# Kernel tuning notes

Hardware: AMD Instinct MI355X
Metric: run time of the kernel (lower is better)

The kernel has to match this reference:

```python
import jax, jax.numpy as jnp
import numpy as np

N_NODES = 100000
N_EDGES = 3200000


def setup_inputs() -> dict:
    key = jax.random.key(0)
    ks = jax.random.split(key, 20)
    x = jax.random.normal(ks[0], (N_NODES, 3), dtype=jnp.float32)
    edge_index = jax.random.randint(ks[1], (2, N_EDGES), 0, N_NODES, dtype=jnp.int64)

    def w(k, shape, fan_in):
        return jax.random.normal(k, shape, dtype=jnp.float32) * (1.0 / np.sqrt(fan_in))

    return {
        "x": x, "edge_index": edge_index,
        # layer 1: in=3, out=16, heads=2
        "W1": w(ks[2], (3, 32), 3), "a_src1": w(ks[3], (2, 16), 16), "a_dst1": w(ks[4], (2, 16), 16), "b1": jnp.zeros((32,), jnp.float32),
        # layer 2: in=32, out=16, heads=2
        "W2": w(ks[5], (32, 32), 32), "a_src2": w(ks[6], (2, 16), 16), "a_dst2": w(ks[7], (2, 16), 16), "b2": jnp.zeros((32,), jnp.float32),
        # layer 3: in=32, out=16, heads=1
        "W3": w(ks[8], (32, 16), 32), "a_src3": w(ks[9], (1, 16), 16), "a_dst3": w(ks[10], (1, 16), 16), "b3": jnp.zeros((16,), jnp.float32),
        # output linear 16 -> 1
        "Wout": w(ks[11], (16, 1), 16), "bout": jnp.zeros((1,), jnp.float32),
    }


def gat_layer(x, src, dst, W, a_src, a_dst, b, heads, ch, n):
    # h: [N, H, C]
    h = (x @ W).reshape(n, heads, ch)
    alpha_src = jnp.sum(h * a_src[None], axis=-1)  # [N, H]
    alpha_dst = jnp.sum(h * a_dst[None], axis=-1)  # [N, H]
    e = jax.nn.leaky_relu(alpha_src[src] + alpha_dst[dst], 0.2)  # [E, H]
    # segment softmax over incoming edges of each dst node
    m = jax.ops.segment_max(e, dst, num_segments=n)
    m = jnp.where(jnp.isfinite(m), m, 0.0)
    ex = jnp.exp(e - jax.lax.stop_gradient(m)[dst])
    s = jax.ops.segment_sum(ex, dst, num_segments=n)
    alpha = ex / (s[dst] + 1e-16)  # [E, H]
    out = jax.ops.segment_sum(h[src] * alpha[:, :, None], dst, num_segments=n)  # [N, H, C]
    return out.reshape(n, heads * ch) + b


def reference(x, edge_index, W1, a_src1, a_dst1, b1, W2, a_src2, a_dst2, b2,
              W3, a_src3, a_dst3, b3, Wout, bout):
    n = x.shape[0]
    loops = jnp.arange(n, dtype=edge_index.dtype)
    src = jnp.concatenate([edge_index[0], loops])  # PyG add_self_loops=True
    dst = jnp.concatenate([edge_index[1], loops])
    h = jax.nn.elu(gat_layer(x, src, dst, W1, a_src1, a_dst1, b1, 2, 16, n))
    h = jax.nn.elu(gat_layer(h, src, dst, W2, a_src2, a_dst2, b2, 2, 16, n))
    h = jax.nn.elu(gat_layer(h, src, dst, W3, a_src3, a_dst3, b3, 1, 16, n))
    embeddings = h
    out = jax.nn.sigmoid(h @ Wout + bout)
    return out, embeddings
```

## Files before the change

kernel.cpp:

```cpp
#include <hip/hip_runtime.h>
#include <hip/hip_fp16.h>
#include <math.h>

#define TPB 256
#define PMAX 128
#define PSH 10
#define PW  1024
#define CHUNK 2048
#define KPT 8
#define PCAP 49152
#define PCSTR 16

__device__ __forceinline__ float leaky02(float x) { return x > 0.f ? x : 0.2f * x; }
__device__ __forceinline__ float eluf(float x) { return x > 0.f ? x : (__expf(x) - 1.f); }


__global__ void zero_kernel(int* __restrict__ p, int n) {
  int i = blockIdx.x * blockDim.x + threadIdx.x;
  if (i < n) p[i] = 0;
}

__global__ __launch_bounds__(256) void scatter_kernel(const int* __restrict__ src,
                                                      const int* __restrict__ dst,
                                                      int E, int n,
                                                      int* __restrict__ pcursor,
                                                      unsigned* __restrict__ pstage) {
  __shared__ int lcnt[4][PMAX];
  __shared__ int ltot[PMAX];
  __shared__ int lscan[PMAX];
  __shared__ int lbase[PMAX];
  __shared__ int wtot;
  __shared__ unsigned slab[CHUNK];
  int t = threadIdx.x;
  int wid = t >> 6;
  int lane = t & 63;
  int Etot = E + n;
  int c0 = blockIdx.x * CHUNK;
  if (c0 >= Etot) return;
  int c1 = min(c0 + CHUNK, Etot);
  for (int j = t; j < 4 * PMAX; j += TPB) ((int*)lcnt)[j] = 0;

  int dd[KPT], ss[KPT];
  bool vv[KPT];
#pragma unroll
  for (int k = 0; k < KPT; ++k) {
    int idx = c0 + t + k * TPB;
    vv[k] = idx < c1;
    if (vv[k]) {
      if (idx < E) { ss[k] = src[idx]; dd[k] = dst[idx]; }
      else         { ss[k] = dd[k] = idx - E; }
    } else { ss[k] = 0; dd[k] = 0; }
  }
  __syncthreads();
#pragma unroll
  for (int k = 0; k < KPT; ++k)
    if (vv[k]) atomicAdd(&lcnt[wid][dd[k] >> PSH], 1);
  __syncthreads();
  int tot = 0, x = 0;
  if (t < PMAX) {
    int a0 = lcnt[0][t], a1 = lcnt[1][t], a2 = lcnt[2][t], a3 = lcnt[3][t];
    tot = a0 + a1 + a2 + a3;
    ltot[t] = tot;
    lcnt[0][t] = 0; lcnt[1][t] = a0; lcnt[2][t] = a0 + a1; lcnt[3][t] = a0 + a1 + a2;
    x = tot;
#pragma unroll
    for (int off = 1; off < 64; off <<= 1) {
      int u = __shfl_up(x, off);
      if (lane >= off) x += u;
    }
    if (t == 63) wtot = x;
  }
  __syncthreads();
  if (t < PMAX) {
    lscan[t] = x - tot + ((t >= 64) ? wtot : 0);
    lbase[t] = tot ? atomicAdd(&pcursor[t * PCSTR], tot) : 0;
  }
  __syncthreads();
#pragma unroll
  for (int k = 0; k < KPT; ++k) {
    if (vv[k]) {
      int p = dd[k] >> PSH;
      int sub = atomicAdd(&lcnt[wid][p], 1);
      slab[lscan[p] + sub] = ((unsigned)ss[k] << PSH) | (unsigned)(dd[k] & (PW - 1));
    }
  }
  __syncthreads();
  for (int p = wid; p < PMAX; p += 4) {
    int cnt = ltot[p];
    int s = lscan[p];
    size_t b = (size_t)p * PCAP + lbase[p];
    for (int j = lane; j < cnt; j += 64)
      pstage[b + j] = slab[s + j];
  }
}

__global__ __launch_bounds__(1024) void build_csr_kernel(const unsigned* __restrict__ pstage,
                                                         const int* __restrict__ pcursor,
                                                         int nvtx,
                                                         int* __restrict__ rowptr,
                                                         int* __restrict__ csr_src) {
  __shared__ int ssum[PMAX];
  __shared__ int lhist[PW];
  __shared__ int lcur[PW];
  int t = threadIdx.x;
  int lane = t & 63;
  int wid = t >> 6;
  int p = blockIdx.x;
  size_t rbase = (size_t)p * PCAP;
  if (t < PMAX) ssum[t] = pcursor[t * PCSTR];
  lhist[t] = 0;
  __syncthreads();
  for (int off = 1; off < PMAX; off <<= 1) {
    int a = 0;
    if (t < PMAX && t >= off) a = ssum[t - off];
    __syncthreads();
    if (t < PMAX) ssum[t] += a;
    __syncthreads();
  }
  int cnt = pcursor[p * PCSTR];
  int wbase = ssum[p] - cnt;
  int nodebase = p << PSH;
  for (int i = t; i < cnt; i += 4096) {
    unsigned w[4]; bool vv[4];
#pragma unroll
    for (int k = 0; k < 4; ++k) {
      int j = i + k * 1024;
      vv[k] = j < cnt;
      w[k] = vv[k] ? pstage[rbase + j] : 0u;
    }
#pragma unroll
    for (int k = 0; k < 4; ++k)
      if (vv[k]) atomicAdd(&lhist[w[k] & (PW - 1)], 1);
  }
  __syncthreads();
  int v = lhist[t];
  int x = v;
#pragma unroll
  for (int off = 1; off < 64; off <<= 1) {
    int u = __shfl_up(x, off);
    if (lane >= off) x += u;
  }
  if (lane == 63) lcur[wid] = x;
  __syncthreads();
  if (t < 16) {
    int wsum = lcur[t];
    int y = wsum;
#pragma unroll
    for (int off = 1; off < 16; off <<= 1) {
      int u = __shfl_up(y, off);
      if (t >= off) y += u;
    }
    lcur[t] = y - wsum;
  }
  __syncthreads();
  int acc = wbase + x + lcur[wid] - v;
  __syncthreads();
  lcur[t] = acc;
  int node = nodebase + t;
  if (node < nvtx) rowptr[node] = acc;
  __syncthreads();
  for (int i = t; i < cnt; i += 4096) {
    unsigned w[4]; bool vv[4];
#pragma unroll
    for (int k = 0; k < 4; ++k) {
      int j = i + k * 1024;
      vv[k] = j < cnt;
      w[k] = vv[k] ? pstage[rbase + j] : 0u;
    }
#pragma unroll
    for (int k = 0; k < 4; ++k) {
      if (vv[k]) {
        int pos = atomicAdd(&lcur[w[k] & (PW - 1)], 1);
        csr_src[pos] = (int)(w[k] >> PSH);
      }
    }
  }
  if (p == (int)gridDim.x - 1 && t == 0) rowptr[nvtx] = wbase + cnt;
}


template<int IN, int OUT, int H>
__global__ void transform_kernel(const float* __restrict__ x, const float* __restrict__ W,
                                 const float* __restrict__ a_src, const float* __restrict__ a_dst,
                                 __half* __restrict__ h, float* __restrict__ asrc,
                                 float* __restrict__ adst, int n) {
  __shared__ float sW[IN * OUT];
  __shared__ float sa[2 * OUT];
  for (int i = threadIdx.x; i < IN * OUT; i += blockDim.x) sW[i] = W[i];
  if (threadIdx.x < OUT) {
    sa[threadIdx.x] = a_src[threadIdx.x];
    sa[OUT + threadIdx.x] = a_dst[threadIdx.x];
  }
  __syncthreads();
  int i = blockIdx.x * blockDim.x + threadIdx.x;
  if (i >= n) return;
  float xv[IN];
#pragma unroll
  for (int k = 0; k < IN; k++) xv[k] = x[(size_t)i * IN + k];
  float hv[OUT];
#pragma unroll
  for (int j = 0; j < OUT; j++) {
    float acc = 0.f;
#pragma unroll
    for (int k = 0; k < IN; k++) acc += xv[k] * sW[k * OUT + j];
    hv[j] = acc;
  }
#pragma unroll
  for (int j = 0; j < OUT; j += 2)
    ((__half2*)h)[((size_t)i * OUT + j) >> 1] = __floats2half2_rn(hv[j], hv[j + 1]);
#pragma unroll
  for (int hh = 0; hh < H; hh++) {
    float as = 0.f, ad = 0.f;
#pragma unroll
    for (int c = 0; c < 16; c++) {
      as += hv[hh * 16 + c] * sa[hh * 16 + c];
      ad += hv[hh * 16 + c] * sa[OUT + hh * 16 + c];
    }
    asrc[i * H + hh] = as;
    adst[i * H + hh] = ad;
  }
}


__global__ __launch_bounds__(256) void node_gat12(
    const int* __restrict__ rowptr,
    const int* __restrict__ csr_src,
    const float* __restrict__ asrc,
    const float* __restrict__ adst,
    const __half* __restrict__ hfeat,
    const float* __restrict__ bias,
    float* __restrict__ outb,
    int n) {
  __shared__ float4 s_e[4][64];
  int wid = threadIdx.x >> 6;
  int lane = threadIdx.x & 63;
  int i = (blockIdx.x * blockDim.x + threadIdx.x) >> 6;
  if (i >= n) return;
  int start = rowptr[i];
  int d = rowptr[i + 1] - start;
  float ad0 = adst[i * 2 + 0];
  float ad1 = adst[i * 2 + 1];
  const uint2* hfp = (const uint2*)hfeat;
  const float2* asrc2 = (const float2*)asrc;
  int g = lane >> 3;
  int q = lane & 7;
  const float2* sp = (const float2*)(&s_e[wid][0]) + (q >> 2);
  float4 acc = make_float4(0.f, 0.f, 0.f, 0.f);
  float sl0 = 0.f, sl1 = 0.f;

  if (d <= 64) {
    int sidx8 = 0;
    float w0 = 0.f, w1 = 0.f;
    if (lane < d) {
      int sidx = csr_src[start + lane];
      sidx8 = sidx << 3;
      float2 av = asrc2[sidx];
      w0 = __expf(leaky02(av.x + ad0));
      w1 = __expf(leaky02(av.y + ad1));
    }
    sl0 = w0; sl1 = w1;
    s_e[wid][lane] = make_float4(__int_as_float(sidx8), w0, __int_as_float(sidx8), w1);
    float2 p[8];
#pragma unroll
    for (int it = 0; it < 8; ++it) p[it] = sp[2 * (g + it * 8)];
    uint2 hv[8];
#pragma unroll
    for (int it = 0; it < 8; ++it) hv[it] = hfp[__float_as_int(p[it].x) + q];
#pragma unroll
    for (int it = 0; it < 8; ++it) {
      float2 fa = __half22float2(*(const __half2*)&hv[it].x);
      float2 fb = __half22float2(*(const __half2*)&hv[it].y);
      float w = p[it].y;
      acc.x += w * fa.x; acc.y += w * fa.y;
      acc.z += w * fb.x; acc.w += w * fb.y;
    }
  } else {
    for (int base = 0; base < d; base += 64) {
      int k = base + lane;
      int sidx8 = 0;
      float w0 = 0.f, w1 = 0.f;
      if (k < d) {
        int sidx = csr_src[start + k];
        sidx8 = sidx << 3;
        float2 av = asrc2[sidx];
        w0 = __expf(leaky02(av.x + ad0));
        w1 = __expf(leaky02(av.y + ad1));
        sl0 += w0; sl1 += w1;
      }
      s_e[wid][lane] = make_float4(__int_as_float(sidx8), w0, __int_as_float(sidx8), w1);
      float2 p[8];
#pragma unroll
      for (int it = 0; it < 8; ++it) p[it] = sp[2 * (g + it * 8)];
      uint2 hv[8];
#pragma unroll
      for (int it = 0; it < 8; ++it) hv[it] = hfp[__float_as_int(p[it].x) + q];
#pragma unroll
      for (int it = 0; it < 8; ++it) {
        float2 fa = __half22float2(*(const __half2*)&hv[it].x);
        float2 fb = __half22float2(*(const __half2*)&hv[it].y);
        float w = p[it].y;
        acc.x += w * fa.x; acc.y += w * fa.y;
        acc.z += w * fb.x; acc.w += w * fb.y;
      }
    }
  }

#pragma unroll
  for (int off = 32; off >= 1; off >>= 1) {
    sl0 += __shfl_xor(sl0, off);
    sl1 += __shfl_xor(sl1, off);
  }
#pragma unroll
  for (int off = 8; off <= 32; off <<= 1) {
    acc.x += __shfl_xor(acc.x, off);
    acc.y += __shfl_xor(acc.y, off);
    acc.z += __shfl_xor(acc.z, off);
    acc.w += __shfl_xor(acc.w, off);
  }
  if (lane < 8) {
    float inv = 1.f / (((lane >= 4) ? sl1 : sl0) + 1e-16f);
    float4 bv = ((const float4*)bias)[lane];
    float4 o;
    o.x = eluf(acc.x * inv + bv.x);
    o.y = eluf(acc.y * inv + bv.y);
    o.z = eluf(acc.z * inv + bv.z);
    o.w = eluf(acc.w * inv + bv.w);
    ((float4*)outb)[(size_t)i * 8 + lane] = o;
  }
}

__global__ __launch_bounds__(256) void node_gat3(
    const int* __restrict__ rowptr,
    const int* __restrict__ csr_src,
    const float* __restrict__ asrc,
    const float* __restrict__ adst,
    const __half* __restrict__ hfeat,
    const float* __restrict__ b3,
    const float* __restrict__ Wout,
    const float* __restrict__ bout,
    float* __restrict__ out,
    int n) {
  __shared__ float2 s_hw[4][64];
  int wid = threadIdx.x >> 6;
  int lane = threadIdx.x & 63;
  int i = (blockIdx.x * blockDim.x + threadIdx.x) >> 6;
  if (i >= n) return;
  int start = rowptr[i];
  int d = rowptr[i + 1] - start;
  float ad0 = adst[i];
  const uint2* hfp = (const uint2*)hfeat;
  int g = lane >> 2;
  int q = lane & 3;
  const float2* sp = s_hw[wid];
  float4 acc = make_float4(0.f, 0.f, 0.f, 0.f);
  float sl = 0.f;

  if (d <= 64) {
    int sidx4 = 0;
    float w0 = 0.f;
    if (lane < d) {
      int sidx = csr_src[start + lane];
      sidx4 = sidx << 2;
      w0 = __expf(leaky02(asrc[sidx] + ad0));
    }
    sl = w0;
    s_hw[wid][lane] = make_float2(__int_as_float(sidx4), w0);
    float2 p[4];
#pragma unroll
    for (int it = 0; it < 4; ++it) p[it] = sp[g + it * 16];
    uint2 hv[4];
#pragma unroll
    for (int it = 0; it < 4; ++it) hv[it] = hfp[__float_as_int(p[it].x) + q];
#pragma unroll
    for (int it = 0; it < 4; ++it) {
      float2 fa = __half22float2(*(const __half2*)&hv[it].x);
      float2 fb = __half22float2(*(const __half2*)&hv[it].y);
      float w = p[it].y;
      acc.x += w * fa.x; acc.y += w * fa.y;
      acc.z += w * fb.x; acc.w += w * fb.y;
    }
  } else {
    for (int base = 0; base < d; base += 64) {
      int k = base + lane;
      int sidx4 = 0;
      float w0 = 0.f;
      if (k < d) {
        int sidx = csr_src[start + k];
        sidx4 = sidx << 2;
        w0 = __expf(leaky02(asrc[sidx] + ad0));
        sl += w0;
      }
      s_hw[wid][lane] = make_float2(__int_as_float(sidx4), w0);
      float2 p[4];
#pragma unroll
      for (int it = 0; it < 4; ++it) p[it] = sp[g + it * 16];
      uint2 hv[4];
#pragma unroll
      for (int it = 0; it < 4; ++it) hv[it] = hfp[__float_as_int(p[it].x) + q];
#pragma unroll
      for (int it = 0; it < 4; ++it) {
        float2 fa = __half22float2(*(const __half2*)&hv[it].x);
        float2 fb = __half22float2(*(const __half2*)&hv[it].y);
        float w = p[it].y;
        acc.x += w * fa.x; acc.y += w * fa.y;
        acc.z += w * fb.x; acc.w += w * fb.y;
      }
    }
  }

#pragma unroll
  for (int off = 32; off >= 1; off >>= 1) sl += __shfl_xor(sl, off);
#pragma unroll
  for (int off = 4; off <= 32; off <<= 1) {
    acc.x += __shfl_xor(acc.x, off);
    acc.y += __shfl_xor(acc.y, off);
    acc.z += __shfl_xor(acc.z, off);
    acc.w += __shfl_xor(acc.w, off);
  }
  float z = 0.f;
  if (lane < 4) {
    float inv = 1.f / (sl + 1e-16f);
    float4 bv = ((const float4*)b3)[lane];
    float4 wv = ((const float4*)Wout)[lane];
    float4 o;
    o.x = eluf(acc.x * inv + bv.x);
    o.y = eluf(acc.y * inv + bv.y);
    o.z = eluf(acc.z * inv + bv.z);
    o.w = eluf(acc.w * inv + bv.w);
    ((float4*)(out + n))[(size_t)i * 4 + lane] = o;
    z = o.x * wv.x + o.y * wv.y + o.z * wv.z + o.w * wv.w;
  }
  z += __shfl_xor(z, 1);
  z += __shfl_xor(z, 2);
  if (lane == 0) out[i] = 1.f / (1.f + __expf(-(z + bout[0])));
}


extern "C" void kernel_launch(void* const* d_in, const int* in_sizes, int n_in,
                              void* d_out, int out_size, void* d_ws, size_t ws_size,
                              hipStream_t stream) {
  const float* x    = (const float*)d_in[0];
  const int*   ei   = (const int*)d_in[1];
  const float* W1   = (const float*)d_in[2];
  const float* as1  = (const float*)d_in[3];
  const float* ad1  = (const float*)d_in[4];
  const float* b1   = (const float*)d_in[5];
  const float* W2   = (const float*)d_in[6];
  const float* as2  = (const float*)d_in[7];
  const float* ad2  = (const float*)d_in[8];
  const float* b2   = (const float*)d_in[9];
  const float* W3   = (const float*)d_in[10];
  const float* as3  = (const float*)d_in[11];
  const float* ad3  = (const float*)d_in[12];
  const float* b3   = (const float*)d_in[13];
  const float* Wout = (const float*)d_in[14];
  const float* bout = (const float*)d_in[15];
  float* out = (float*)d_out;

  const int n = in_sizes[0] / 3;
  const int E = in_sizes[1] / 2;
  const int Etot = E + n;
  const int* src = ei;
  const int* dst = ei + E;
  const int nbC = (Etot + CHUNK - 1) / CHUNK;
  const int NP = ((n - 1) >> PSH) + 1;

  float* ws = (float*)d_ws;
  float* bufH = ws;
  float* bufX = bufH + (size_t)n * 32;
  float* asrc = bufX + (size_t)n * 32;
  float* adst = asrc + (size_t)n * 2;
  int* rowptr  = (int*)(adst + (size_t)n * 2);
  int* pcursor = rowptr + n + 1;
  int* csr_src = pcursor + PMAX * PCSTR;
  unsigned* pstage = (unsigned*)ws;
  __half* hH = (__half*)bufH;

  const int nbN = (n + TPB - 1) / TPB;
  const int nbW = (n + 3) / 4;

  zero_kernel<<<(PMAX * PCSTR + TPB - 1) / TPB, TPB, 0, stream>>>(pcursor, PMAX * PCSTR);
  scatter_kernel<<<nbC, TPB, 0, stream>>>(src, dst, E, n, pcursor, pstage);
  build_csr_kernel<<<NP, 1024, 0, stream>>>(pstage, pcursor, n, rowptr, csr_src);

  transform_kernel<3, 32, 2><<<nbN, TPB, 0, stream>>>(x, W1, as1, ad1, hH, asrc, adst, n);
  node_gat12<<<nbW, TPB, 0, stream>>>(rowptr, csr_src, asrc, adst, hH, b1, bufX, n);

  transform_kernel<32, 32, 2><<<nbN, TPB, 0, stream>>>(bufX, W2, as2, ad2, hH, asrc, adst, n);
  node_gat12<<<nbW, TPB, 0, stream>>>(rowptr, csr_src, asrc, adst, hH, b2, bufX, n);

  transform_kernel<32, 16, 1><<<nbN, TPB, 0, stream>>>(bufX, W3, as3, ad3, hH, asrc, adst, n);
  node_gat3<<<nbW, TPB, 0, stream>>>(rowptr, csr_src, asrc, adst, hH, b3, Wout, bout, out, n);
}
```

Before: 360.3 us.

## Regroup layer-3 gather to 8 lanes per edge, shrink PCAP, use memset for cursors

Result: no change. 361.8 us (+0.4%).

```diff
diff --git a/kernel.cpp b/kernel.cpp
--- a/kernel.cpp
+++ b/kernel.cpp
@@ -8,17 +8,12 @@
 #define PW  1024
 #define CHUNK 2048
 #define KPT 8
-#define PCAP 49152
+#define PCAP 38912
 #define PCSTR 16
 
 __device__ __forceinline__ float leaky02(float x) { return x > 0.f ? x : 0.2f * x; }
 __device__ __forceinline__ float eluf(float x) { return x > 0.f ? x : (__expf(x) - 1.f); }
 
-
-__global__ void zero_kernel(int* __restrict__ p, int n) {
-  int i = blockIdx.x * blockDim.x + threadIdx.x;
-  if (i < n) p[i] = 0;
-}
 
 __global__ __launch_bounds__(256) void scatter_kernel(const int* __restrict__ src,
                                                       const int* __restrict__ dst,
@@ -348,62 +343,58 @@
   int start = rowptr[i];
   int d = rowptr[i + 1] - start;
   float ad0 = adst[i];
-  const uint2* hfp = (const uint2*)hfeat;
-  int g = lane >> 2;
-  int q = lane & 3;
+  const unsigned* hfp = (const unsigned*)hfeat;
+  int g = lane >> 3;
+  int q = lane & 7;
   const float2* sp = s_hw[wid];
-  float4 acc = make_float4(0.f, 0.f, 0.f, 0.f);
+  float2 acc = make_float2(0.f, 0.f);
   float sl = 0.f;
 
   if (d <= 64) {
-    int sidx4 = 0;
+    int sidx8 = 0;
     float w0 = 0.f;
     if (lane < d) {
       int sidx = csr_src[start + lane];
-      sidx4 = sidx << 2;
+      sidx8 = sidx << 3;
       w0 = __expf(leaky02(asrc[sidx] + ad0));
     }
     sl = w0;
-    s_hw[wid][lane] = make_float2(__int_as_float(sidx4), w0);
-    float2 p[4];
-#pragma unroll
-    for (int it = 0; it < 4; ++it) p[it] = sp[g + it * 16];
-    uint2 hv[4];
-#pragma unroll
-    for (int it = 0; it < 4; ++it) hv[it] = hfp[__float_as_int(p[it].x) + q];
-#pragma unroll
-    for (int it = 0; it < 4; ++it) {
-      float2 fa = __half22float2(*(const __half2*)&hv[it].x);
-      float2 fb = __half22float2(*(const __half2*)&hv[it].y);
+    s_hw[wid][lane] = make_float2(__int_as_float(sidx8), w0);
+    float2 p[8];
+#pragma unroll
+    for (int it = 0; it < 8; ++it) p[it] = sp[g + it * 8];
+    unsigned hv[8];
+#pragma unroll
+    for (int it = 0; it < 8; ++it) hv[it] = hfp[__float_as_int(p[it].x) + q];
+#pragma unroll
+    for (int it = 0; it < 8; ++it) {
+      float2 f = __half22float2(*(const __half2*)&hv[it]);
       float w = p[it].y;
-      acc.x += w * fa.x; acc.y += w * fa.y;
-      acc.z += w * fb.x; acc.w += w * fb.y;
+      acc.x += w * f.x; acc.y += w * f.y;
     }
   } else {
     for (int base = 0; base < d; base += 64) {
       int k = base + lane;
-      int sidx4 = 0;
+      int sidx8 = 0;
       float w0 = 0.f;
       if (k < d) {
         int sidx = csr_src[start + k];
-        sidx4 = sidx << 2;
+        sidx8 = sidx << 3;
         w0 = __expf(leaky02(asrc[sidx] + ad0));
         sl += w0;
       }
-      s_hw[wid][lane] = make_float2(__int_as_float(sidx4), w0);
-      float2 p[4];
-#pragma unroll
-      for (int it = 0; it < 4; ++it) p[it] = sp[g + it * 16];
-      uint2 hv[4];
-#pragma unroll
-      for (int it = 0; it < 4; ++it) hv[it] = hfp[__float_as_int(p[it].x) + q];
-#pragma unroll
-      for (int it = 0; it < 4; ++it) {
-        float2 fa = __half22float2(*(const __half2*)&hv[it].x);
-        float2 fb = __half22float2(*(const __half2*)&hv[it].y);
+      s_hw[wid][lane] = make_float2(__int_as_float(sidx8), w0);
+      float2 p[8];
+#pragma unroll
+      for (int it = 0; it < 8; ++it) p[it] = sp[g + it * 8];
+      unsigned hv[8];
+#pragma unroll
+      for (int it = 0; it < 8; ++it) hv[it] = hfp[__float_as_int(p[it].x) + q];
+#pragma unroll
+      for (int it = 0; it < 8; ++it) {
+        float2 f = __half22float2(*(const __half2*)&hv[it]);
         float w = p[it].y;
-        acc.x += w * fa.x; acc.y += w * fa.y;
-        acc.z += w * fb.x; acc.w += w * fb.y;
+        acc.x += w * f.x; acc.y += w * f.y;
       }
     }
   }
@@ -411,27 +402,24 @@
 #pragma unroll
   for (int off = 32; off >= 1; off >>= 1) sl += __shfl_xor(sl, off);
 #pragma unroll
-  for (int off = 4; off <= 32; off <<= 1) {
+  for (int off = 8; off <= 32; off <<= 1) {
     acc.x += __shfl_xor(acc.x, off);
     acc.y += __shfl_xor(acc.y, off);
-    acc.z += __shfl_xor(acc.z, off);
-    acc.w += __shfl_xor(acc.w, off);
   }
   float z = 0.f;
-  if (lane < 4) {
+  if (lane < 8) {
     float inv = 1.f / (sl + 1e-16f);
-    float4 bv = ((const float4*)b3)[lane];
-    float4 wv = ((const float4*)Wout)[lane];
-    float4 o;
+    float2 bv = ((const float2*)b3)[lane];
+    float2 wv = ((const float2*)Wout)[lane];
+    float2 o;
     o.x = eluf(acc.x * inv + bv.x);
     o.y = eluf(acc.y * inv + bv.y);
-    o.z = eluf(acc.z * inv + bv.z);
-    o.w = eluf(acc.w * inv + bv.w);
-    ((float4*)(out + n))[(size_t)i * 4 + lane] = o;
-    z = o.x * wv.x + o.y * wv.y + o.z * wv.z + o.w * wv.w;
+    ((float2*)(out + n))[(size_t)i * 8 + lane] = o;
+    z = o.x * wv.x + o.y * wv.y;
   }
   z += __shfl_xor(z, 1);
   z += __shfl_xor(z, 2);
+  z += __shfl_xor(z, 4);
   if (lane == 0) out[i] = 1.f / (1.f + __expf(-(z + bout[0])));
 }
 
@@ -479,7 +467,7 @@
   const int nbN = (n + TPB - 1) / TPB;
   const int nbW = (n + 3) / 4;
 
-  zero_kernel<<<(PMAX * PCSTR + TPB - 1) / TPB, TPB, 0, stream>>>(pcursor, PMAX * PCSTR);
+  hipMemsetAsync(pcursor, 0, PMAX * PCSTR * sizeof(int), stream);
   scatter_kernel<<<nbC, TPB, 0, stream>>>(src, dst, E, n, pcursor, pstage);
   build_csr_kernel<<<NP, 1024, 0, stream>>>(pstage, pcursor, n, rowptr, csr_src);
 
```
